# Kernel tuning notes

Measured on AMD Instinct MI355X. Metric: run time of the kernel, lower is better.

The kernel has to match this reference:

```python
import jax, jax.numpy as jnp
import numpy as np

# Geometry constants hardcoded in the torch module
B, H, W = 1, 256, 256
A, DC = 64, 1024            # n_views, det_count
NSAMP = 512                  # samples per ray for the line integral
DSRC, DDET, SPACING = 500.0, 500.0, 2.0
NPAD = 2048                  # fft padding (next pow2 >= 2*DC)
FEAT = 32


def _bilinear_image(img, px, py):
    """Bilinear sample img (B,H,W) at centered coords px,py (any shape). Zero outside."""
    b, hh, ww = img.shape
    cx = px + (ww - 1) / 2.0
    cy = py + (hh - 1) / 2.0
    x0 = jnp.floor(cx); y0 = jnp.floor(cy)
    fx = cx - x0; fy = cy - y0
    x0i = x0.astype(jnp.int32); y0i = y0.astype(jnp.int32)
    flat = img.reshape(b, -1)

    def gather(yi, xi):
        valid = (yi >= 0) & (yi < hh) & (xi >= 0) & (xi < ww)
        yc = jnp.clip(yi, 0, hh - 1); xc = jnp.clip(xi, 0, ww - 1)
        idx = (yc * ww + xc).reshape(-1)
        v = jnp.take(flat, idx, axis=1).reshape((b,) + yi.shape)
        return v * valid.astype(img.dtype)

    return (gather(y0i, x0i) * (1 - fx) * (1 - fy)
            + gather(y0i, x0i + 1) * fx * (1 - fy)
            + gather(y0i + 1, x0i) * (1 - fx) * fy
            + gather(y0i + 1, x0i + 1) * fx * fy)


def fan_forward(img, theta):
    """Ray-driven fan-beam forward projection. img (B,1,H,W) -> sino (B,A,DC)."""
    im = img[:, 0]
    c = jnp.cos(theta); s = jnp.sin(theta)
    src = DSRC * jnp.stack([c, s], -1)                    # (A,2) source positions
    e = jnp.stack([-s, c], -1)                            # detector axis
    u = (jnp.arange(DC) - (DC - 1) / 2.0) * SPACING       # detector offsets
    det = -DDET * jnp.stack([c, s], -1)[:, None, :] + u[None, :, None] * e[:, None, :]  # (A,DC,2)
    d = det - src[:, None, :]
    L = jnp.sqrt(jnp.sum(d * d, axis=-1))                 # (A,DC) ray lengths
    t = (jnp.arange(NSAMP, dtype=jnp.float32) + 0.5) / NSAMP
    pts = src[:, None, None, :] + t[None, None, :, None] * d[:, :, None, :]  # (A,DC,N,2)
    vals = _bilinear_image(im, pts[..., 0], pts[..., 1])  # (B,A,DC,N)
    return jnp.sum(vals, axis=-1) * (L / NSAMP)[None]


def filter_sinogram(sino):
    """Ram-Lak ramp filtering along the detector axis with zero-padding."""
    f = jnp.abs(jnp.fft.rfftfreq(NPAD)).astype(jnp.float32)  # cycles/sample
    sf = jnp.fft.rfft(sino, n=NPAD, axis=-1) * (2.0 * f)
    return jnp.fft.irfft(sf, n=NPAD, axis=-1)[..., :DC].astype(sino.dtype)


def fan_backprojection(sino, theta):
    """Pixel-driven fan-beam backprojection. sino (B,A,DC) -> (B,1,H,W)."""
    xs = jnp.arange(W, dtype=jnp.float32) - (W - 1) / 2.0
    ys = jnp.arange(H, dtype=jnp.float32) - (H - 1) / 2.0
    gx, gy = jnp.meshgrid(xs, ys)                         # (H,W)
    c = jnp.cos(theta)[:, None, None]; s = jnp.sin(theta)[:, None, None]
    xr = gx[None] * c + gy[None] * s                      # (A,H,W) rotated coords
    yr = -gx[None] * s + gy[None] * c
    denom = DSRC - xr
    uu = yr * (DSRC + DDET) / denom                       # detector coordinate
    wgt = (DSRC * DSRC) / (denom * denom)                 # fan-beam distance weight
    iu = uu / SPACING + (DC - 1) / 2.0
    i0 = jnp.floor(iu); fr = iu - i0
    i0i = i0.astype(jnp.int32)
    aidx = jnp.arange(A)[:, None, None]
    b = sino.shape[0]
    flat = sino.reshape(b, -1)

    def g(ii):
        valid = (ii >= 0) & (ii < DC)
        ic = jnp.clip(ii, 0, DC - 1)
        idx = (aidx * DC + ic).reshape(-1)
        v = jnp.take(flat, idx, axis=1).reshape((b, A, H, W))
        return v * valid.astype(sino.dtype)

    vals = g(i0i) * (1 - fr) + g(i0i + 1) * fr            # (B,A,H,W)
    bp = jnp.sum(vals * wgt[None], axis=1) * (jnp.pi / A)
    return bp[:, None]


def conv(x, w):
    return jax.lax.conv_general_dilated(x, w, (1, 1), 'SAME',
                                        dimension_numbers=('NCHW', 'OIHW', 'NCHW'))


def setup_inputs():
    key = jax.random.key(0)
    ks = jax.random.split(key, 8)
    x = jax.random.normal(ks[0], (B, 1, H, W), jnp.float32)
    theta = jnp.arange(A, dtype=jnp.float32) * (2.0 * np.pi / A)
    sinogram = jax.random.normal(ks[1], (B, A, DC), jnp.float32)

    def xav(k, shape):
        fan_in = shape[1] * 9; fan_out = shape[0] * 9
        return jax.random.normal(k, shape, jnp.float32) * np.sqrt(2.0 / (fan_in + fan_out)).astype(np.float32)

    return {
        'x': x, 'theta': theta, 'sinogram': sinogram,
        'lambda_step': jnp.float32(0.5), 'soft_thr': jnp.float32(0.01),
        'conv1_forward': xav(ks[2], (FEAT, 1, 3, 3)),
        'conv2_forward': xav(ks[3], (FEAT, FEAT, 3, 3)),
        'conv1_backward': xav(ks[4], (FEAT, FEAT, 3, 3)),
        'conv2_backward': xav(ks[5], (1, FEAT, 3, 3)),
    }


def reference(x, theta, sinogram, lambda_step, soft_thr,
              conv1_forward, conv2_forward, conv1_backward, conv2_backward):
    sino_pred = fan_forward(x, theta)
    filtered = filter_sinogram(sino_pred)
    X_fbp = fan_backprojection(filtered - sinogram, theta)
    x_input = x - lambda_step * X_fbp
    h = jax.nn.relu(conv(x_input, conv1_forward))
    x_forward = conv(h, conv2_forward)
    hs = jnp.sign(x_forward) * jax.nn.relu(jnp.abs(x_forward) - soft_thr)
    x_pred = conv(jax.nn.relu(conv(hs, conv1_backward)), conv2_backward)
    x_est = conv(jax.nn.relu(conv(x_forward, conv1_backward)), conv2_backward)
    symloss = x_est - x_input
    return (x_pred, symloss)
```

## Files before the change

kernel.cpp:

```cpp
#include <hip/hip_runtime.h>

#define DEV_INLINE __device__ __forceinline__

#define PI_F 3.14159265358979323846f

#define H_OFF     0
#define SINO_OFF  2048
#define DIFF_OFF  67584
#define XIN_OFF   133120
#define WF2F_OFF  198656
#define WF1B_OFF  207872
#define WF2B_OFF  212480
#define BUFA_OFF  217088
#define BUFB_OFF  2314240

typedef short bf16x8 __attribute__((ext_vector_type(8)));
typedef float f32x4 __attribute__((ext_vector_type(4)));

union FragI4 { int4 i4; bf16x8 v; };
union I4U    { int4 i4; int i[4]; };

DEV_INLINE unsigned rne1(float a) {
  unsigned u = __float_as_uint(a);
  return (u + 0x7FFFu + ((u >> 16) & 1u)) >> 16;
}
DEV_INLINE int pack_rne(float a, float b) {
  return (int)(rne1(a) | (rne1(b) << 16));
}

__global__ __launch_bounds__(256) void setup_kernel(
    const float* __restrict__ sino_in, const float* __restrict__ w2f,
    const float* __restrict__ w1b, const float* __restrict__ w2b,
    const float* __restrict__ img,
    float* __restrict__ h, float* __restrict__ diff,
    int* __restrict__ wf2f, int* __restrict__ wf1b, int* __restrict__ wf2b,
    float4* __restrict__ quadP) {
  const int b = blockIdx.x;
  const int tid = threadIdx.x;
  if (b < 64) {
    __shared__ float hp[8][32];
    const int cell = tid & 31;
    const int kq = tid >> 5;
    const int n = b * 32 + cell;
    float ssum = 0.0f;
    const float ang_scale = PI_F / 1024.0f;
    for (int k = kq * 128; k < kq * 128 + 128; ++k) {
      int m = (k * n) & 2047;
      ssum += (float)k * __cosf((float)m * ang_scale);
    }
    hp[kq][cell] = ssum;
    __syncthreads();
    if (tid < 32) {
      float S = 0.0f;
      #pragma unroll
      for (int q = 0; q < 8; ++q) S += hp[q][tid];
      int nn = b * 32 + tid;
      float sgn = (nn & 1) ? -1.0f : 1.0f;
      h[nn] = (S * (1.0f / 512.0f) + sgn) * (1.0f / 2048.0f);
    }
  } else if (b < 320) {
    int idx = (b - 64) * 256 + tid;
    diff[idx] = -sino_in[idx];
  } else if (b < 356) {
    const bool second = (b >= 338);
    int idx = (b - (second ? 338 : 320)) * 256 + tid;
    int d = idx & 3;
    int L = (idx >> 2) & 63;
    int jm = idx >> 8;
    int j = jm >> 1, mt = jm & 1;
    int co = mt * 16 + (L & 15);
    int ci0 = (L >> 4) * 8 + 2 * d;
    const float* w = second ? w1b : w2f;
    int v = pack_rne(w[co * 288 + ci0 * 9 + j], w[co * 288 + (ci0 + 1) * 9 + j]);
    (second ? wf1b : wf2f)[idx] = v;
  } else if (b < 617) {
    int idx = (b - 356) * 256 + tid;
    if (idx < 258 * 258) {
      int y = idx / 258;
      int x = idx - y * 258;
      float4 v;
      int ay = y - 1, bx = x - 1;
      bool y0ok = (ay >= 0 && ay < 256);
      bool y1ok = (ay + 1 >= 0 && ay + 1 < 256);
      bool x0ok = (bx >= 0 && bx < 256);
      bool x1ok = (bx + 1 >= 0 && bx + 1 < 256);
      v.x = (y0ok && x0ok) ? img[(ay << 8) + bx] : 0.0f;
      v.y = (y0ok && x1ok) ? img[(ay << 8) + bx + 1] : 0.0f;
      v.z = (y1ok && x0ok) ? img[((ay + 1) << 8) + bx] : 0.0f;
      v.w = (y1ok && x1ok) ? img[((ay + 1) << 8) + bx + 1] : 0.0f;
      quadP[idx] = v;
    }
  } else {
    int d = tid & 3;
    int L = tid >> 2;
    int n = L & 15;
    int k0 = (L >> 4) * 8 + 2 * d;
    float lo = (n < 9) ? w2b[k0 * 9 + n] : 0.0f;
    float hi = (n < 9) ? w2b[(k0 + 1) * 9 + n] : 0.0f;
    wf2b[tid] = pack_rne(lo, hi);
  }
}

__global__ __launch_bounds__(256) void fwdproj(
    const float4* __restrict__ quadP, const float* __restrict__ theta,
    float* __restrict__ sino) {
  __shared__ float part[8][32];
  __shared__ float cs[2];
  const int tid = threadIdx.x;
  const int a = blockIdx.x >> 5;
  const int cell = tid & 31;
  const int chunk = tid >> 5;
  const int d = ((blockIdx.x & 31) << 5) + cell;
  if (tid == 0) {
    float th = theta[a];
    cs[0] = cosf(th);
    cs[1] = sinf(th);
  }
  __syncthreads();
  const float c = cs[0], s = cs[1];
  const float u = ((float)d - 511.5f) * 2.0f;
  const float dxv = -1000.0f * c - u * s;
  const float dyv = -1000.0f * s + u * c;
  const float L = sqrtf(1.0e6f + u * u);
  const float sx = fmaf(500.0f, c, 127.5f);
  const float sy = fmaf(500.0f, s, 127.5f);

  float tlo = 0.0f, thi = 1.0f;
  if (fabsf(dxv) > 1e-6f) {
    float inv = 1.0f / dxv;
    float a0 = (-1.0f - sx) * inv, a1 = (256.0f - sx) * inv;
    tlo = fmaxf(tlo, fminf(a0, a1));
    thi = fminf(thi, fmaxf(a0, a1));
  } else if (sx <= -1.0f || sx >= 256.0f) {
    thi = -1.0f;
  }
  if (fabsf(dyv) > 1e-6f) {
    float inv = 1.0f / dyv;
    float a0 = (-1.0f - sy) * inv, a1 = (256.0f - sy) * inv;
    tlo = fmaxf(tlo, fminf(a0, a1));
    thi = fminf(thi, fmaxf(a0, a1));
  } else if (sy <= -1.0f || sy >= 256.0f) {
    thi = -1.0f;
  }
  int imin = (int)ceilf(tlo * 512.0f - 0.5f) - 1;
  imin = imin < 0 ? 0 : imin;
  int imax = (int)floorf(thi * 512.0f - 0.5f) + 1;
  imax = imax > 511 ? 511 : imax;

  float acc = 0.0f;
  int i = imin + chunk;
  for (; i + 8 <= imax; i += 16) {
    float t0 = ((float)i + 0.5f) * (1.0f / 512.0f);
    float cx0 = fmaf(t0, dxv, sx);
    float cy0 = fmaf(t0, dyv, sy);
    cx0 = fminf(fmaxf(cx0, -1.0f), 256.0f);
    cy0 = fminf(fmaxf(cy0, -1.0f), 256.0f);
    float xf0 = floorf(cx0), yf0 = floorf(cy0);
    float fx0 = cx0 - xf0, fy0 = cy0 - yf0;
    int idx0 = ((int)yf0 + 1) * 258 + (int)xf0 + 1;
    float t1 = ((float)(i + 8) + 0.5f) * (1.0f / 512.0f);
    float cx1 = fmaf(t1, dxv, sx);
    float cy1 = fmaf(t1, dyv, sy);
    cx1 = fminf(fmaxf(cx1, -1.0f), 256.0f);
    cy1 = fminf(fmaxf(cy1, -1.0f), 256.0f);
    float xf1 = floorf(cx1), yf1 = floorf(cy1);
    float fx1 = cx1 - xf1, fy1 = cy1 - yf1;
    int idx1 = ((int)yf1 + 1) * 258 + (int)xf1 + 1;
    float4 q0 = quadP[idx0];
    float4 q1 = quadP[idx1];
    {
      float gx = 1.0f - fx0, gy = 1.0f - fy0;
      acc += gy * (gx * q0.x + fx0 * q0.y) + fy0 * (gx * q0.z + fx0 * q0.w);
    }
    {
      float gx = 1.0f - fx1, gy = 1.0f - fy1;
      acc += gy * (gx * q1.x + fx1 * q1.y) + fy1 * (gx * q1.z + fx1 * q1.w);
    }
  }
  if (i <= imax) {
    float t = ((float)i + 0.5f) * (1.0f / 512.0f);
    float cx = fmaf(t, dxv, sx);
    float cy = fmaf(t, dyv, sy);
    cx = fminf(fmaxf(cx, -1.0f), 256.0f);
    cy = fminf(fmaxf(cy, -1.0f), 256.0f);
    float xf = floorf(cx), yf = floorf(cy);
    float fx = cx - xf, fy = cy - yf;
    int ix = (int)xf + 1;
    int iy = (int)yf + 1;
    float4 q = quadP[iy * 258 + ix];
    float gx = 1.0f - fx, gy = 1.0f - fy;
    acc += gy * (gx * q.x + fx * q.y) + fy * (gx * q.z + fx * q.w);
  }
  part[chunk][cell] = acc;
  __syncthreads();
  if (tid < 32) {
    float r = 0.0f;
    #pragma unroll
    for (int q = 0; q < 8; ++q) r += part[q][tid];
    sino[a * 1024 + ((blockIdx.x & 31) << 5) + tid] = r * (L * (1.0f / 512.0f));
  }
}

__global__ __launch_bounds__(256) void filt(
    const float* __restrict__ sino_pred, const float* __restrict__ h,
    float* __restrict__ diff) {
  __shared__ __align__(16) float srow[256];
  __shared__ __align__(16) float hextW[1288];
  const int a = blockIdx.x >> 2;
  const int q = blockIdx.x & 3;
  const int tid = threadIdx.x;
  const int k0base = q * 256;
  srow[tid] = sino_pred[a * 1024 + k0base + tid];
  const int shift = 259 + k0base;
  for (int m = tid; m < 1288; m += 256) hextW[m] = h[(m - shift) & 2047];
  __syncthreads();
  const int dd0 = tid * 4;
  float acc0 = 0.f, acc1 = 0.f, acc2 = 0.f, acc3 = 0.f;
  #pragma unroll 4
  for (int kk = 0; kk < 256; kk += 4) {
    float4 sv = *reinterpret_cast<const float4*>(&srow[kk]);
    int mb = dd0 + 256 - kk;
    float4 hA = *reinterpret_cast<const float4*>(&hextW[mb]);
    float4 hB = *reinterpret_cast<const float4*>(&hextW[mb + 4]);
    acc0 = fmaf(sv.x, hA.w, acc0); acc0 = fmaf(sv.y, hA.z, acc0);
    acc0 = fmaf(sv.z, hA.y, acc0); acc0 = fmaf(sv.w, hA.x, acc0);
    acc1 = fmaf(sv.x, hB.x, acc1); acc1 = fmaf(sv.y, hA.w, acc1);
    acc1 = fmaf(sv.z, hA.z, acc1); acc1 = fmaf(sv.w, hA.y, acc1);
    acc2 = fmaf(sv.x, hB.y, acc2); acc2 = fmaf(sv.y, hB.x, acc2);
    acc2 = fmaf(sv.z, hA.w, acc2); acc2 = fmaf(sv.w, hA.z, acc2);
    acc3 = fmaf(sv.x, hB.z, acc3); acc3 = fmaf(sv.y, hB.y, acc3);
    acc3 = fmaf(sv.z, hB.x, acc3); acc3 = fmaf(sv.w, hA.w, acc3);
  }
  float* o = diff + a * 1024 + dd0;
  atomicAdd(o + 0, acc0);
  atomicAdd(o + 1, acc1);
  atomicAdd(o + 2, acc2);
  atomicAdd(o + 3, acc3);
}

__global__ __launch_bounds__(512) void backproj(
    const float* __restrict__ diff, const float* __restrict__ theta,
    const float* __restrict__ lam_p, const float* __restrict__ img,
    float* __restrict__ x_input) {
  __shared__ float cst[64], snt[64];
  __shared__ float part[512];
  const int tid = threadIdx.x;
  if (tid < 64) {
    float th = theta[tid];
    cst[tid] = cosf(th);
    snt[tid] = sinf(th);
  }
  __syncthreads();
  const int tX = (blockIdx.x & 7) << 5;
  const int tY = (blockIdx.x >> 3) << 2;
  const int pl = tid & 127;
  const int ag = tid >> 7;
  const int pxi = tX + (pl & 31);
  const int pyi = tY + (pl >> 5);
  const float gx = (float)pxi - 127.5f;
  const float gy = (float)pyi - 127.5f;
  float acc = 0.0f;
  for (int ai = ag * 16; ai < ag * 16 + 16; ++ai) {
    float c = cst[ai], s = snt[ai];
    float xr = gx * c + gy * s;
    float yr = gy * c - gx * s;
    float denom = 500.0f - xr;
    float inv = 1.0f / denom;
    float uu = yr * 1000.0f * inv;
    float wgt = 250000.0f * inv * inv;
    float iu = uu * 0.5f + 511.5f;
    float i0f = floorf(iu);
    float fr = iu - i0f;
    int i0 = (int)i0f;
    int c0 = min(max(i0, 0), 1023);
    int c1 = min(max(i0 + 1, 0), 1023);
    float m0 = (i0 >= 0 && i0 < 1024) ? 1.0f : 0.0f;
    float m1 = (i0 + 1 >= 0 && i0 + 1 < 1024) ? 1.0f : 0.0f;
    const float* row = diff + ai * 1024;
    float v0 = row[c0] * m0;
    float v1 = row[c1] * m1;
    acc += (v0 * (1.0f - fr) + v1 * fr) * wgt;
  }
  part[tid] = acc;
  __syncthreads();
  if (tid < 128) {
    float sum = part[tid] + part[tid + 128] + part[tid + 256] + part[tid + 384];
    int p = ((tY + (tid >> 5)) << 8) + tX + (tid & 31);
    x_input[p] = img[p] - lam_p[0] * 0.04908738521234052f * sum;
  }
}

__global__ __launch_bounds__(256) void conv12f(
    const float* __restrict__ x_input, const float* __restrict__ w1f,
    const int* __restrict__ wf2f, int* __restrict__ xfp) {
  __shared__ float xin[8][36];
  __shared__ __align__(16) int htile[3264];
  const int tid = threadIdx.x;
  const int lane = tid & 63;
  const int wave = tid >> 6;
  const int tX = (blockIdx.x & 7) << 5;
  const int tY = (blockIdx.x >> 3) << 2;

  FragI4 wf[2][9];
  const int4* wfg = (const int4*)wf2f;
  #pragma unroll
  for (int mt = 0; mt < 2; ++mt)
    #pragma unroll
    for (int j = 0; j < 9; ++j) wf[mt][j].i4 = wfg[(j * 2 + mt) * 64 + lane];

  for (int idx = tid; idx < 288; idx += 256) {
    int sy = idx / 36;
    int sx = idx - sy * 36;
    int gy = tY + sy - 2, gx = tX + sx - 2;
    xin[sy][sx] = (gy >= 0 && gy < 256 && gx >= 0 && gx < 256)
                      ? x_input[(gy << 8) + gx] : 0.0f;
  }
  __syncthreads();

  for (int pos = tid; pos < 204; pos += 256) {
    int yy = pos / 34;
    int xx = pos - yy * 34;
    int hy = tY + yy - 1, hx = tX + xx - 1;
    bool hin = (hy >= 0 && hy < 256 && hx >= 0 && hx < 256);
    float v[9];
    #pragma unroll
    for (int dy = 0; dy < 3; ++dy)
      #pragma unroll
      for (int dx = 0; dx < 3; ++dx) v[dy * 3 + dx] = xin[yy + dy][xx + dx];
    int packs[16];
    #pragma unroll
    for (int c2 = 0; c2 < 16; ++c2) {
      float r0 = 0.0f, r1 = 0.0f;
      #pragma unroll
      for (int j = 0; j < 9; ++j) {
        r0 = fmaf(v[j], w1f[(2 * c2) * 9 + j], r0);
        r1 = fmaf(v[j], w1f[(2 * c2 + 1) * 9 + j], r1);
      }
      r0 = hin ? fmaxf(r0, 0.0f) : 0.0f;
      r1 = hin ? fmaxf(r1, 0.0f) : 0.0f;
      packs[c2] = pack_rne(r0, r1);
    }
    #pragma unroll
    for (int g = 0; g < 4; ++g)
      *reinterpret_cast<int4*>(&htile[g * 816 + pos * 4]) =
          make_int4(packs[4 * g], packs[4 * g + 1],
                    packs[4 * g + 2], packs[4 * g + 3]);
  }
  __syncthreads();

  const int y = wave;
  const int n = lane & 15;
  const int q = lane >> 4;
  const int qb = q * 816;
  for (int xt = 0; xt < 2; ++xt) {
    const int x0 = xt << 4;
    f32x4 acc0 = {0.f, 0.f, 0.f, 0.f};
    f32x4 acc1 = {0.f, 0.f, 0.f, 0.f};
    #pragma unroll
    for (int j = 0; j < 9; ++j) {
      int dy = j / 3, dx = j - dy * 3;
      int pb = (y + dy) * 34 + x0 + dx + n;
      FragI4 bf;
      bf.i4 = *reinterpret_cast<const int4*>(&htile[qb + pb * 4]);
      acc0 = __builtin_amdgcn_mfma_f32_16x16x32_bf16(wf[0][j].v, bf.v, acc0, 0, 0, 0);
      acc1 = __builtin_amdgcn_mfma_f32_16x16x32_bf16(wf[1][j].v, bf.v, acc1, 0, 0, 0);
    }
    const int gpos = ((tY + y) << 8) + tX + x0 + n;
    int2* xp = (int2*)(xfp + (gpos << 4));
    xp[q]     = make_int2(pack_rne(acc0[0], acc0[1]), pack_rne(acc0[2], acc0[3]));
    xp[4 + q] = make_int2(pack_rne(acc1[0], acc1[1]), pack_rne(acc1[2], acc1[3]));
  }
}

__global__ __launch_bounds__(256) void branch_tail(
    const int* __restrict__ xfp, const int* __restrict__ wf1b,
    const int* __restrict__ wf2b, const float* __restrict__ thr_p,
    const float* __restrict__ x_input, float* __restrict__ out) {
  __shared__ __align__(16) int ldsX[8704];
  __shared__ __align__(16) int ldsD[6400];
  float* ldsP = (float*)ldsX;
  const int tid = threadIdx.x;
  const int lane = tid & 63;
  const int wave = tid >> 6;
  const int branch = blockIdx.x >> 8;
  const int tileb = blockIdx.x & 255;
  const int tX = (tileb & 3) << 6;
  const int tY = (tileb >> 2) << 2;
  const float thr = thr_p[0];
  const bool soft = (branch == 0);

  FragI4 wf[2][9];
  const int4* wfg = (const int4*)wf1b;
  #pragma unroll
  for (int mt = 0; mt < 2; ++mt)
    #pragma unroll
    for (int j = 0; j < 9; ++j) wf[mt][j].i4 = wfg[(j * 2 + mt) * 64 + lane];
  FragI4 wb;
  wb.i4 = ((const int4*)wf2b)[lane];

  if (tid < 16) {
    int g = tid >> 2, px = 396 + (tid & 3);
    *reinterpret_cast<int4*>(&ldsD[g * 1600 + px * 4]) = make_int4(0, 0, 0, 0);
  }

  #pragma unroll
  for (int t = 0; t < 3; ++t) {
    int p = tid + t * 256;
    if (p < 544) {
      int sy = p / 68;
      int sx = p - sy * 68;
      int gy = tY + sy - 2, gx = tX + sx - 2;
      bool ok = ((unsigned)gy < 256u) && ((unsigned)gx < 256u);
      I4U w[4];
      if (ok) {
        const int4* src = (const int4*)(xfp + (((gy << 8) + gx) << 4));
        w[0].i4 = src[0]; w[1].i4 = src[1]; w[2].i4 = src[2]; w[3].i4 = src[3];
      } else {
        w[0].i4 = w[1].i4 = w[2].i4 = w[3].i4 = make_int4(0, 0, 0, 0);
      }
      #pragma unroll
      for (int g = 0; g < 4; ++g) {
        if (soft) {
          #pragma unroll
          for (int k = 0; k < 4; ++k) {
            int v = w[g].i[k];
            float lo = __uint_as_float(((unsigned)v) << 16);
            float hi = __uint_as_float(((unsigned)v) & 0xFFFF0000u);
            lo = fmaxf(lo - thr, 0.0f) + fminf(lo + thr, 0.0f);
            hi = fmaxf(hi - thr, 0.0f) + fminf(hi + thr, 0.0f);
            w[g].i[k] = pack_rne(lo, hi);
          }
        }
        *reinterpret_cast<int4*>(&ldsX[g * 2176 + p * 4]) = w[g].i4;
      }
    }
  }
  __syncthreads();

  const int n = lane & 15;
  const int q = lane >> 4;
  const int rxtab[5] = {-1, 15, 31, 47, 49};
  for (int t = wave; t < 30; t += 4) {
    int trow = t / 5;
    int ry = trow - 1;
    int rx0 = rxtab[t - trow * 5];
    int rxn = rx0 + n;
    bool inimg = ((unsigned)(tX + rxn) < 256u) && ((unsigned)(tY + ry) < 256u);
    int pxD = (ry + 1) * 66 + rxn + 1;
    f32x4 acc0 = {0.f, 0.f, 0.f, 0.f};
    f32x4 acc1 = {0.f, 0.f, 0.f, 0.f};
    #pragma unroll
    for (int j = 0; j < 9; ++j) {
      int dy = j / 3, dx = j - dy * 3;
      int pb = (ry + 1 + dy) * 68 + rx0 + 1 + dx + n;
      FragI4 bf;
      bf.i4 = *reinterpret_cast<const int4*>(&ldsX[q * 2176 + pb * 4]);
      acc0 = __builtin_amdgcn_mfma_f32_16x16x32_bf16(wf[0][j].v, bf.v, acc0, 0, 0, 0);
      acc1 = __builtin_amdgcn_mfma_f32_16x16x32_bf16(wf[1][j].v, bf.v, acc1, 0, 0, 0);
    }
    float a00 = inimg ? fmaxf(acc0[0], 0.0f) : 0.0f;
    float a01 = inimg ? fmaxf(acc0[1], 0.0f) : 0.0f;
    float a02 = inimg ? fmaxf(acc0[2], 0.0f) : 0.0f;
    float a03 = inimg ? fmaxf(acc0[3], 0.0f) : 0.0f;
    float a10 = inimg ? fmaxf(acc1[0], 0.0f) : 0.0f;
    float a11 = inimg ? fmaxf(acc1[1], 0.0f) : 0.0f;
    float a12 = inimg ? fmaxf(acc1[2], 0.0f) : 0.0f;
    float a13 = inimg ? fmaxf(acc1[3], 0.0f) : 0.0f;
    *reinterpret_cast<int2*>(
        &ldsD[(q >> 1) * 1600 + pxD * 4 + (q & 1) * 2]) =
        make_int2(pack_rne(a00, a01), pack_rne(a02, a03));
    *reinterpret_cast<int2*>(
        &ldsD[(2 + (q >> 1)) * 1600 + pxD * 4 + (q & 1) * 2]) =
        make_int2(pack_rne(a10, a11), pack_rne(a12, a13));
  }
  __syncthreads();

  for (int t = wave; t < 25; t += 4) {
    int pbase = t << 4;
    FragI4 af;
    af.i4 = *reinterpret_cast<const int4*>(&ldsD[q * 1600 + (pbase + n) * 4]);
    f32x4 acc = {0.f, 0.f, 0.f, 0.f};
    acc = __builtin_amdgcn_mfma_f32_16x16x32_bf16(af.v, wb.v, acc, 0, 0, 0);
    #pragma unroll
    for (int r = 0; r < 4; ++r)
      ldsP[(pbase + q * 4 + r) * 17 + n] = acc[r];
  }
  __syncthreads();

  const int px = tid & 63, py = tid >> 6;
  float acc = 0.0f;
  #pragma unroll
  for (int j = 0; j < 9; ++j) {
    int dy = j / 3, dx = j - dy * 3;
    int rp = (py + dy) * 66 + px + dx;
    acc += ldsP[rp * 17 + j];
  }
  const int p = ((tY + py) << 8) + tX + px;
  if (branch == 0) out[p] = acc;
  else out[65536 + p] = acc - x_input[p];
}

extern "C" void kernel_launch(void* const* d_in, const int* in_sizes, int n_in,
                              void* d_out, int out_size, void* d_ws, size_t ws_size,
                              hipStream_t stream) {
  const float* x       = (const float*)d_in[0];
  const float* theta   = (const float*)d_in[1];
  const float* sino_in = (const float*)d_in[2];
  const float* lam     = (const float*)d_in[3];
  const float* thr     = (const float*)d_in[4];
  const float* w_c1f   = (const float*)d_in[5];
  const float* w_c2f   = (const float*)d_in[6];
  const float* w_c1b   = (const float*)d_in[7];
  const float* w_c2b   = (const float*)d_in[8];
  float* out = (float*)d_out;
  float* ws  = (float*)d_ws;

  float* h         = ws + H_OFF;
  float* sino_pred = ws + SINO_OFF;
  float* diff      = ws + DIFF_OFF;
  float* x_input   = ws + XIN_OFF;
  int*   wf2f      = (int*)(ws + WF2F_OFF);
  int*   wf1b      = (int*)(ws + WF1B_OFF);
  int*   wf2b      = (int*)(ws + WF2B_OFF);
  float4* quadP    = (float4*)(ws + BUFA_OFF);
  int*   xfp       = (int*)(ws + BUFB_OFF);

  setup_kernel<<<618, 256, 0, stream>>>(sino_in, w_c2f, w_c1b, w_c2b, x, h,
                                        diff, wf2f, wf1b, wf2b, quadP);
  fwdproj<<<2048, 256, 0, stream>>>(quadP, theta, sino_pred);
  filt<<<256, 256, 0, stream>>>(sino_pred, h, diff);
  backproj<<<512, 512, 0, stream>>>(diff, theta, lam, x, x_input);
  conv12f<<<512, 256, 0, stream>>>(x_input, w_c1f, wf2f, xfp);
  branch_tail<<<512, 256, 0, stream>>>(xfp, wf1b, wf2b, thr, x_input, out);
}
```

Before: 127.4 us.

## Fuse filter, backprojection and conv stages into one cooperative kernel with grid syncs

Replaces the four tail kernels (ramp filter, backprojection, first conv pair, branch tail) with a single cooperative kernel of 256 blocks of 512 threads that separates stages with grid.sync(). Each block now handles two tiles per stage, and both branches are processed sequentially within a block. The goal is to remove kernel launch gaps and per-kernel ramp overhead. In exchange it drops to 256 blocks, leaves half the threads idle in some phases, and carries grid-barrier cost plus a large shared-memory footprint that limits occupancy.

Result: slower. 226.3 us (+77.7%).

```diff
diff --git a/kernel.cpp b/kernel.cpp
--- a/kernel.cpp
+++ b/kernel.cpp
@@ -1,7 +1,9 @@
 #include <hip/hip_runtime.h>
+#include <hip/hip_cooperative_groups.h>
+
+namespace cg = cooperative_groups;
 
 #define DEV_INLINE __device__ __forceinline__
-
 #define PI_F 3.14159265358979323846f
 
 #define H_OFF     0
@@ -201,303 +203,326 @@
   }
 }
 
-__global__ __launch_bounds__(256) void filt(
-    const float* __restrict__ sino_pred, const float* __restrict__ h,
-    float* __restrict__ diff) {
-  __shared__ __align__(16) float srow[256];
-  __shared__ __align__(16) float hextW[1288];
-  const int a = blockIdx.x >> 2;
-  const int q = blockIdx.x & 3;
+__global__ __launch_bounds__(512) void fused_tail(
+    const float* __restrict__ img, const float* __restrict__ theta,
+    const float* __restrict__ lam_p, const float* __restrict__ thr_p,
+    const float* __restrict__ w1f, const int* __restrict__ wf2f,
+    const int* __restrict__ wf1b, const int* __restrict__ wf2b,
+    const float* __restrict__ hbuf, const float* __restrict__ sino,
+    float* __restrict__ diff, float* __restrict__ x_input,
+    int* __restrict__ xfp, float* __restrict__ out) {
+  __shared__ __align__(16) int U[15104];
+  cg::grid_group grid = cg::this_grid();
+  const int b = blockIdx.x;
   const int tid = threadIdx.x;
-  const int k0base = q * 256;
-  srow[tid] = sino_pred[a * 1024 + k0base + tid];
-  const int shift = 259 + k0base;
-  for (int m = tid; m < 1288; m += 256) hextW[m] = h[(m - shift) & 2047];
-  __syncthreads();
-  const int dd0 = tid * 4;
-  float acc0 = 0.f, acc1 = 0.f, acc2 = 0.f, acc3 = 0.f;
-  #pragma unroll 4
-  for (int kk = 0; kk < 256; kk += 4) {
-    float4 sv = *reinterpret_cast<const float4*>(&srow[kk]);
-    int mb = dd0 + 256 - kk;
-    float4 hA = *reinterpret_cast<const float4*>(&hextW[mb]);
-    float4 hB = *reinterpret_cast<const float4*>(&hextW[mb + 4]);
-    acc0 = fmaf(sv.x, hA.w, acc0); acc0 = fmaf(sv.y, hA.z, acc0);
-    acc0 = fmaf(sv.z, hA.y, acc0); acc0 = fmaf(sv.w, hA.x, acc0);
-    acc1 = fmaf(sv.x, hB.x, acc1); acc1 = fmaf(sv.y, hA.w, acc1);
-    acc1 = fmaf(sv.z, hA.z, acc1); acc1 = fmaf(sv.w, hA.y, acc1);
-    acc2 = fmaf(sv.x, hB.y, acc2); acc2 = fmaf(sv.y, hB.x, acc2);
-    acc2 = fmaf(sv.z, hA.w, acc2); acc2 = fmaf(sv.w, hA.z, acc2);
-    acc3 = fmaf(sv.x, hB.z, acc3); acc3 = fmaf(sv.y, hB.y, acc3);
-    acc3 = fmaf(sv.z, hB.x, acc3); acc3 = fmaf(sv.w, hA.w, acc3);
-  }
-  float* o = diff + a * 1024 + dd0;
-  atomicAdd(o + 0, acc0);
-  atomicAdd(o + 1, acc1);
-  atomicAdd(o + 2, acc2);
-  atomicAdd(o + 3, acc3);
-}
-
-__global__ __launch_bounds__(512) void backproj(
-    const float* __restrict__ diff, const float* __restrict__ theta,
-    const float* __restrict__ lam_p, const float* __restrict__ img,
-    float* __restrict__ x_input) {
-  __shared__ float cst[64], snt[64];
-  __shared__ float part[512];
-  const int tid = threadIdx.x;
-  if (tid < 64) {
-    float th = theta[tid];
-    cst[tid] = cosf(th);
-    snt[tid] = sinf(th);
-  }
-  __syncthreads();
-  const int tX = (blockIdx.x & 7) << 5;
-  const int tY = (blockIdx.x >> 3) << 2;
-  const int pl = tid & 127;
-  const int ag = tid >> 7;
-  const int pxi = tX + (pl & 31);
-  const int pyi = tY + (pl >> 5);
-  const float gx = (float)pxi - 127.5f;
-  const float gy = (float)pyi - 127.5f;
-  float acc = 0.0f;
-  for (int ai = ag * 16; ai < ag * 16 + 16; ++ai) {
-    float c = cst[ai], s = snt[ai];
-    float xr = gx * c + gy * s;
-    float yr = gy * c - gx * s;
-    float denom = 500.0f - xr;
-    float inv = 1.0f / denom;
-    float uu = yr * 1000.0f * inv;
-    float wgt = 250000.0f * inv * inv;
-    float iu = uu * 0.5f + 511.5f;
-    float i0f = floorf(iu);
-    float fr = iu - i0f;
-    int i0 = (int)i0f;
-    int c0 = min(max(i0, 0), 1023);
-    int c1 = min(max(i0 + 1, 0), 1023);
-    float m0 = (i0 >= 0 && i0 < 1024) ? 1.0f : 0.0f;
-    float m1 = (i0 + 1 >= 0 && i0 + 1 < 1024) ? 1.0f : 0.0f;
-    const float* row = diff + ai * 1024;
-    float v0 = row[c0] * m0;
-    float v1 = row[c1] * m1;
-    acc += (v0 * (1.0f - fr) + v1 * fr) * wgt;
-  }
-  part[tid] = acc;
-  __syncthreads();
-  if (tid < 128) {
-    float sum = part[tid] + part[tid + 128] + part[tid + 256] + part[tid + 384];
-    int p = ((tY + (tid >> 5)) << 8) + tX + (tid & 31);
-    x_input[p] = img[p] - lam_p[0] * 0.04908738521234052f * sum;
-  }
-}
-
-__global__ __launch_bounds__(256) void conv12f(
-    const float* __restrict__ x_input, const float* __restrict__ w1f,
-    const int* __restrict__ wf2f, int* __restrict__ xfp) {
-  __shared__ float xin[8][36];
-  __shared__ __align__(16) int htile[3264];
-  const int tid = threadIdx.x;
-  const int lane = tid & 63;
-  const int wave = tid >> 6;
-  const int tX = (blockIdx.x & 7) << 5;
-  const int tY = (blockIdx.x >> 3) << 2;
-
-  FragI4 wf[2][9];
-  const int4* wfg = (const int4*)wf2f;
-  #pragma unroll
-  for (int mt = 0; mt < 2; ++mt)
+
+  {
+    float* srow  = (float*)U;
+    float* hextW = (float*)U + 256;
+    const int a = b >> 2;
+    const int q = b & 3;
+    const int k0base = q * 256;
+    if (tid < 256) srow[tid] = sino[a * 1024 + k0base + tid];
+    const int shift = 259 + k0base;
+    for (int m = tid; m < 1288; m += 512) hextW[m] = hbuf[(m - shift) & 2047];
+    __syncthreads();
+    if (tid < 256) {
+      const int dd0 = tid * 4;
+      float acc0 = 0.f, acc1 = 0.f, acc2 = 0.f, acc3 = 0.f;
+      #pragma unroll 4
+      for (int kk = 0; kk < 256; kk += 4) {
+        float4 sv = *reinterpret_cast<const float4*>(&srow[kk]);
+        int mb = dd0 + 256 - kk;
+        float4 hA = *reinterpret_cast<const float4*>(&hextW[mb]);
+        float4 hB = *reinterpret_cast<const float4*>(&hextW[mb + 4]);
+        acc0 = fmaf(sv.x, hA.w, acc0); acc0 = fmaf(sv.y, hA.z, acc0);
+        acc0 = fmaf(sv.z, hA.y, acc0); acc0 = fmaf(sv.w, hA.x, acc0);
+        acc1 = fmaf(sv.x, hB.x, acc1); acc1 = fmaf(sv.y, hA.w, acc1);
+        acc1 = fmaf(sv.z, hA.z, acc1); acc1 = fmaf(sv.w, hA.y, acc1);
+        acc2 = fmaf(sv.x, hB.y, acc2); acc2 = fmaf(sv.y, hB.x, acc2);
+        acc2 = fmaf(sv.z, hA.w, acc2); acc2 = fmaf(sv.w, hA.z, acc2);
+        acc3 = fmaf(sv.x, hB.z, acc3); acc3 = fmaf(sv.y, hB.y, acc3);
+        acc3 = fmaf(sv.z, hB.x, acc3); acc3 = fmaf(sv.w, hA.w, acc3);
+      }
+      float* o = diff + a * 1024 + dd0;
+      atomicAdd(o + 0, acc0);
+      atomicAdd(o + 1, acc1);
+      atomicAdd(o + 2, acc2);
+      atomicAdd(o + 3, acc3);
+    }
+  }
+  grid.sync();
+
+  {
+    float* cst  = (float*)U;
+    float* snt  = (float*)U + 64;
+    float* part = (float*)U + 128;
+    if (tid < 64) {
+      float th = theta[tid];
+      cst[tid] = cosf(th);
+      snt[tid] = sinf(th);
+    }
+    __syncthreads();
+    const int tX = (b & 7) << 5;
+    const int tYb = (b >> 3) << 3;
+    const int pl = tid & 127;
+    const int ag = tid >> 7;
+    const float lamc = lam_p[0] * 0.04908738521234052f;
     #pragma unroll
-    for (int j = 0; j < 9; ++j) wf[mt][j].i4 = wfg[(j * 2 + mt) * 64 + lane];
-
-  for (int idx = tid; idx < 288; idx += 256) {
-    int sy = idx / 36;
-    int sx = idx - sy * 36;
-    int gy = tY + sy - 2, gx = tX + sx - 2;
-    xin[sy][sx] = (gy >= 0 && gy < 256 && gx >= 0 && gx < 256)
-                      ? x_input[(gy << 8) + gx] : 0.0f;
-  }
-  __syncthreads();
-
-  for (int pos = tid; pos < 204; pos += 256) {
-    int yy = pos / 34;
-    int xx = pos - yy * 34;
-    int hy = tY + yy - 1, hx = tX + xx - 1;
-    bool hin = (hy >= 0 && hy < 256 && hx >= 0 && hx < 256);
-    float v[9];
+    for (int tt = 0; tt < 2; ++tt) {
+      const int tY = tYb + (tt << 2);
+      const int pxi = tX + (pl & 31);
+      const int pyi = tY + (pl >> 5);
+      const float gx = (float)pxi - 127.5f;
+      const float gy = (float)pyi - 127.5f;
+      float acc = 0.0f;
+      for (int ai = ag * 16; ai < ag * 16 + 16; ++ai) {
+        float c = cst[ai], s = snt[ai];
+        float xr = gx * c + gy * s;
+        float yr = gy * c - gx * s;
+        float denom = 500.0f - xr;
+        float inv = 1.0f / denom;
+        float uu = yr * 1000.0f * inv;
+        float wgt = 250000.0f * inv * inv;
+        float iu = uu * 0.5f + 511.5f;
+        float i0f = floorf(iu);
+        float fr = iu - i0f;
+        int i0 = (int)i0f;
+        int c0 = min(max(i0, 0), 1023);
+        int c1 = min(max(i0 + 1, 0), 1023);
+        float m0 = (i0 >= 0 && i0 < 1024) ? 1.0f : 0.0f;
+        float m1 = (i0 + 1 >= 0 && i0 + 1 < 1024) ? 1.0f : 0.0f;
+        const float* row = diff + ai * 1024;
+        float v0 = row[c0] * m0;
+        float v1 = row[c1] * m1;
+        acc += (v0 * (1.0f - fr) + v1 * fr) * wgt;
+      }
+      part[tid] = acc;
+      __syncthreads();
+      if (tid < 128) {
+        float sum = part[tid] + part[tid + 128] + part[tid + 256] + part[tid + 384];
+        int p = ((tY + (tid >> 5)) << 8) + tX + (tid & 31);
+        x_input[p] = img[p] - lamc * sum;
+      }
+      __syncthreads();
+    }
+  }
+  grid.sync();
+
+  {
+    float (*xin)[36] = (float(*)[36])U;
+    int* htile = U + 288;
+    const int lane = tid & 63;
+    const int wave = tid >> 6;
+    const int tX = (b & 7) << 5;
+    const int tYb = (b >> 3) << 3;
+
+    FragI4 wfr[2][9];
+    const int4* wfg = (const int4*)wf2f;
     #pragma unroll
-    for (int dy = 0; dy < 3; ++dy)
+    for (int mt = 0; mt < 2; ++mt)
       #pragma unroll
-      for (int dx = 0; dx < 3; ++dx) v[dy * 3 + dx] = xin[yy + dy][xx + dx];
-    int packs[16];
+      for (int j = 0; j < 9; ++j) wfr[mt][j].i4 = wfg[(j * 2 + mt) * 64 + lane];
+
     #pragma unroll
-    for (int c2 = 0; c2 < 16; ++c2) {
-      float r0 = 0.0f, r1 = 0.0f;
+    for (int tt = 0; tt < 2; ++tt) {
+      const int tY = tYb + (tt << 2);
+      if (tid < 288) {
+        int sy = tid / 36;
+        int sx = tid - sy * 36;
+        int gy = tY + sy - 2, gx = tX + sx - 2;
+        xin[sy][sx] = (gy >= 0 && gy < 256 && gx >= 0 && gx < 256)
+                          ? x_input[(gy << 8) + gx] : 0.0f;
+      }
+      __syncthreads();
+
+      if (tid < 204) {
+        int pos = tid;
+        int yy = pos / 34;
+        int xx = pos - yy * 34;
+        int hy = tY + yy - 1, hx = tX + xx - 1;
+        bool hin = (hy >= 0 && hy < 256 && hx >= 0 && hx < 256);
+        float v[9];
+        #pragma unroll
+        for (int dy = 0; dy < 3; ++dy)
+          #pragma unroll
+          for (int dx = 0; dx < 3; ++dx) v[dy * 3 + dx] = xin[yy + dy][xx + dx];
+        int packs[16];
+        #pragma unroll
+        for (int c2 = 0; c2 < 16; ++c2) {
+          float r0 = 0.0f, r1 = 0.0f;
+          #pragma unroll
+          for (int j = 0; j < 9; ++j) {
+            r0 = fmaf(v[j], w1f[(2 * c2) * 9 + j], r0);
+            r1 = fmaf(v[j], w1f[(2 * c2 + 1) * 9 + j], r1);
+          }
+          r0 = hin ? fmaxf(r0, 0.0f) : 0.0f;
+          r1 = hin ? fmaxf(r1, 0.0f) : 0.0f;
+          packs[c2] = pack_rne(r0, r1);
+        }
+        #pragma unroll
+        for (int g = 0; g < 4; ++g)
+          *reinterpret_cast<int4*>(&htile[g * 816 + pos * 4]) =
+              make_int4(packs[4 * g], packs[4 * g + 1],
+                        packs[4 * g + 2], packs[4 * g + 3]);
+      }
+      __syncthreads();
+
+      {
+        const int y = wave & 3;
+        const int xt = wave >> 2;
+        const int n = lane & 15;
+        const int q = lane >> 4;
+        const int qb = q * 816;
+        const int x0 = xt << 4;
+        f32x4 acc0 = {0.f, 0.f, 0.f, 0.f};
+        f32x4 acc1 = {0.f, 0.f, 0.f, 0.f};
+        #pragma unroll
+        for (int j = 0; j < 9; ++j) {
+          int dy = j / 3, dx = j - dy * 3;
+          int pb = (y + dy) * 34 + x0 + dx + n;
+          FragI4 bf;
+          bf.i4 = *reinterpret_cast<const int4*>(&htile[qb + pb * 4]);
+          acc0 = __builtin_amdgcn_mfma_f32_16x16x32_bf16(wfr[0][j].v, bf.v, acc0, 0, 0, 0);
+          acc1 = __builtin_amdgcn_mfma_f32_16x16x32_bf16(wfr[1][j].v, bf.v, acc1, 0, 0, 0);
+        }
+        const int gpos = ((tY + y) << 8) + tX + x0 + n;
+        int2* xp = (int2*)(xfp + (gpos << 4));
+        xp[q]     = make_int2(pack_rne(acc0[0], acc0[1]), pack_rne(acc0[2], acc0[3]));
+        xp[4 + q] = make_int2(pack_rne(acc1[0], acc1[1]), pack_rne(acc1[2], acc1[3]));
+      }
+      __syncthreads();
+    }
+  }
+  grid.sync();
+
+  {
+    int* ldsX = U;
+    int* ldsD = U + 8704;
+    float* ldsP = (float*)U;
+    const int lane = tid & 63;
+    const int wave = tid >> 6;
+    const int tX = (b & 3) << 6;
+    const int tY = (b >> 2) << 2;
+    const float thr = thr_p[0];
+
+    FragI4 wfr[2][9];
+    const int4* wfg = (const int4*)wf1b;
+    #pragma unroll
+    for (int mt = 0; mt < 2; ++mt)
       #pragma unroll
-      for (int j = 0; j < 9; ++j) {
-        r0 = fmaf(v[j], w1f[(2 * c2) * 9 + j], r0);
-        r1 = fmaf(v[j], w1f[(2 * c2 + 1) * 9 + j], r1);
-      }
-      r0 = hin ? fmaxf(r0, 0.0f) : 0.0f;
-      r1 = hin ? fmaxf(r1, 0.0f) : 0.0f;
-      packs[c2] = pack_rne(r0, r1);
-    }
-    #pragma unroll
-    for (int g = 0; g < 4; ++g)
-      *reinterpret_cast<int4*>(&htile[g * 816 + pos * 4]) =
-          make_int4(packs[4 * g], packs[4 * g + 1],
-                    packs[4 * g + 2], packs[4 * g + 3]);
-  }
-  __syncthreads();
-
-  const int y = wave;
-  const int n = lane & 15;
-  const int q = lane >> 4;
-  const int qb = q * 816;
-  for (int xt = 0; xt < 2; ++xt) {
-    const int x0 = xt << 4;
-    f32x4 acc0 = {0.f, 0.f, 0.f, 0.f};
-    f32x4 acc1 = {0.f, 0.f, 0.f, 0.f};
-    #pragma unroll
-    for (int j = 0; j < 9; ++j) {
-      int dy = j / 3, dx = j - dy * 3;
-      int pb = (y + dy) * 34 + x0 + dx + n;
-      FragI4 bf;
-      bf.i4 = *reinterpret_cast<const int4*>(&htile[qb + pb * 4]);
-      acc0 = __builtin_amdgcn_mfma_f32_16x16x32_bf16(wf[0][j].v, bf.v, acc0, 0, 0, 0);
-      acc1 = __builtin_amdgcn_mfma_f32_16x16x32_bf16(wf[1][j].v, bf.v, acc1, 0, 0, 0);
-    }
-    const int gpos = ((tY + y) << 8) + tX + x0 + n;
-    int2* xp = (int2*)(xfp + (gpos << 4));
-    xp[q]     = make_int2(pack_rne(acc0[0], acc0[1]), pack_rne(acc0[2], acc0[3]));
-    xp[4 + q] = make_int2(pack_rne(acc1[0], acc1[1]), pack_rne(acc1[2], acc1[3]));
-  }
-}
-
-__global__ __launch_bounds__(256) void branch_tail(
-    const int* __restrict__ xfp, const int* __restrict__ wf1b,
-    const int* __restrict__ wf2b, const float* __restrict__ thr_p,
-    const float* __restrict__ x_input, float* __restrict__ out) {
-  __shared__ __align__(16) int ldsX[8704];
-  __shared__ __align__(16) int ldsD[6400];
-  float* ldsP = (float*)ldsX;
-  const int tid = threadIdx.x;
-  const int lane = tid & 63;
-  const int wave = tid >> 6;
-  const int branch = blockIdx.x >> 8;
-  const int tileb = blockIdx.x & 255;
-  const int tX = (tileb & 3) << 6;
-  const int tY = (tileb >> 2) << 2;
-  const float thr = thr_p[0];
-  const bool soft = (branch == 0);
-
-  FragI4 wf[2][9];
-  const int4* wfg = (const int4*)wf1b;
-  #pragma unroll
-  for (int mt = 0; mt < 2; ++mt)
-    #pragma unroll
-    for (int j = 0; j < 9; ++j) wf[mt][j].i4 = wfg[(j * 2 + mt) * 64 + lane];
-  FragI4 wb;
-  wb.i4 = ((const int4*)wf2b)[lane];
-
-  if (tid < 16) {
-    int g = tid >> 2, px = 396 + (tid & 3);
-    *reinterpret_cast<int4*>(&ldsD[g * 1600 + px * 4]) = make_int4(0, 0, 0, 0);
-  }
-
-  #pragma unroll
-  for (int t = 0; t < 3; ++t) {
-    int p = tid + t * 256;
-    if (p < 544) {
-      int sy = p / 68;
-      int sx = p - sy * 68;
-      int gy = tY + sy - 2, gx = tX + sx - 2;
-      bool ok = ((unsigned)gy < 256u) && ((unsigned)gx < 256u);
-      I4U w[4];
-      if (ok) {
-        const int4* src = (const int4*)(xfp + (((gy << 8) + gx) << 4));
-        w[0].i4 = src[0]; w[1].i4 = src[1]; w[2].i4 = src[2]; w[3].i4 = src[3];
-      } else {
-        w[0].i4 = w[1].i4 = w[2].i4 = w[3].i4 = make_int4(0, 0, 0, 0);
-      }
+      for (int j = 0; j < 9; ++j) wfr[mt][j].i4 = wfg[(j * 2 + mt) * 64 + lane];
+    FragI4 wb;
+    wb.i4 = ((const int4*)wf2b)[lane];
+
+    if (tid < 16) {
+      int g = tid >> 2, px = 396 + (tid & 3);
+      *reinterpret_cast<int4*>(&ldsD[g * 1600 + px * 4]) = make_int4(0, 0, 0, 0);
+    }
+
+    const int n = lane & 15;
+    const int q = lane >> 4;
+    const int rxtab[5] = {-1, 15, 31, 47, 49};
+
+    for (int bb = 0; bb < 2; ++bb) {
+      const bool soft = (bb == 0);
       #pragma unroll
-      for (int g = 0; g < 4; ++g) {
-        if (soft) {
+      for (int t = 0; t < 2; ++t) {
+        int p = tid + t * 512;
+        if (p < 544) {
+          int sy = p / 68;
+          int sx = p - sy * 68;
+          int gy = tY + sy - 2, gx = tX + sx - 2;
+          bool ok = ((unsigned)gy < 256u) && ((unsigned)gx < 256u);
+          I4U w[4];
+          if (ok) {
+            const int4* src = (const int4*)(xfp + (((gy << 8) + gx) << 4));
+            w[0].i4 = src[0]; w[1].i4 = src[1]; w[2].i4 = src[2]; w[3].i4 = src[3];
+          } else {
+            w[0].i4 = w[1].i4 = w[2].i4 = w[3].i4 = make_int4(0, 0, 0, 0);
+          }
           #pragma unroll
-          for (int k = 0; k < 4; ++k) {
-            int v = w[g].i[k];
-            float lo = __uint_as_float(((unsigned)v) << 16);
-            float hi = __uint_as_float(((unsigned)v) & 0xFFFF0000u);
-            lo = fmaxf(lo - thr, 0.0f) + fminf(lo + thr, 0.0f);
-            hi = fmaxf(hi - thr, 0.0f) + fminf(hi + thr, 0.0f);
-            w[g].i[k] = pack_rne(lo, hi);
+          for (int g = 0; g < 4; ++g) {
+            if (soft) {
+              #pragma unroll
+              for (int k = 0; k < 4; ++k) {
+                int v = w[g].i[k];
+                float lo = __uint_as_float(((unsigned)v) << 16);
+                float hi = __uint_as_float(((unsigned)v) & 0xFFFF0000u);
+                lo = fmaxf(lo - thr, 0.0f) + fminf(lo + thr, 0.0f);
+                hi = fmaxf(hi - thr, 0.0f) + fminf(hi + thr, 0.0f);
+                w[g].i[k] = pack_rne(lo, hi);
+              }
+            }
+            *reinterpret_cast<int4*>(&ldsX[g * 2176 + p * 4]) = w[g].i4;
           }
         }
-        *reinterpret_cast<int4*>(&ldsX[g * 2176 + p * 4]) = w[g].i4;
-      }
-    }
-  }
-  __syncthreads();
-
-  const int n = lane & 15;
-  const int q = lane >> 4;
-  const int rxtab[5] = {-1, 15, 31, 47, 49};
-  for (int t = wave; t < 30; t += 4) {
-    int trow = t / 5;
-    int ry = trow - 1;
-    int rx0 = rxtab[t - trow * 5];
-    int rxn = rx0 + n;
-    bool inimg = ((unsigned)(tX + rxn) < 256u) && ((unsigned)(tY + ry) < 256u);
-    int pxD = (ry + 1) * 66 + rxn + 1;
-    f32x4 acc0 = {0.f, 0.f, 0.f, 0.f};
-    f32x4 acc1 = {0.f, 0.f, 0.f, 0.f};
-    #pragma unroll
-    for (int j = 0; j < 9; ++j) {
-      int dy = j / 3, dx = j - dy * 3;
-      int pb = (ry + 1 + dy) * 68 + rx0 + 1 + dx + n;
-      FragI4 bf;
-      bf.i4 = *reinterpret_cast<const int4*>(&ldsX[q * 2176 + pb * 4]);
-      acc0 = __builtin_amdgcn_mfma_f32_16x16x32_bf16(wf[0][j].v, bf.v, acc0, 0, 0, 0);
-      acc1 = __builtin_amdgcn_mfma_f32_16x16x32_bf16(wf[1][j].v, bf.v, acc1, 0, 0, 0);
-    }
-    float a00 = inimg ? fmaxf(acc0[0], 0.0f) : 0.0f;
-    float a01 = inimg ? fmaxf(acc0[1], 0.0f) : 0.0f;
-    float a02 = inimg ? fmaxf(acc0[2], 0.0f) : 0.0f;
-    float a03 = inimg ? fmaxf(acc0[3], 0.0f) : 0.0f;
-    float a10 = inimg ? fmaxf(acc1[0], 0.0f) : 0.0f;
-    float a11 = inimg ? fmaxf(acc1[1], 0.0f) : 0.0f;
-    float a12 = inimg ? fmaxf(acc1[2], 0.0f) : 0.0f;
-    float a13 = inimg ? fmaxf(acc1[3], 0.0f) : 0.0f;
-    *reinterpret_cast<int2*>(
-        &ldsD[(q >> 1) * 1600 + pxD * 4 + (q & 1) * 2]) =
-        make_int2(pack_rne(a00, a01), pack_rne(a02, a03));
-    *reinterpret_cast<int2*>(
-        &ldsD[(2 + (q >> 1)) * 1600 + pxD * 4 + (q & 1) * 2]) =
-        make_int2(pack_rne(a10, a11), pack_rne(a12, a13));
-  }
-  __syncthreads();
-
-  for (int t = wave; t < 25; t += 4) {
-    int pbase = t << 4;
-    FragI4 af;
-    af.i4 = *reinterpret_cast<const int4*>(&ldsD[q * 1600 + (pbase + n) * 4]);
-    f32x4 acc = {0.f, 0.f, 0.f, 0.f};
-    acc = __builtin_amdgcn_mfma_f32_16x16x32_bf16(af.v, wb.v, acc, 0, 0, 0);
-    #pragma unroll
-    for (int r = 0; r < 4; ++r)
-      ldsP[(pbase + q * 4 + r) * 17 + n] = acc[r];
-  }
-  __syncthreads();
-
-  const int px = tid & 63, py = tid >> 6;
-  float acc = 0.0f;
-  #pragma unroll
-  for (int j = 0; j < 9; ++j) {
-    int dy = j / 3, dx = j - dy * 3;
-    int rp = (py + dy) * 66 + px + dx;
-    acc += ldsP[rp * 17 + j];
-  }
-  const int p = ((tY + py) << 8) + tX + px;
-  if (branch == 0) out[p] = acc;
-  else out[65536 + p] = acc - x_input[p];
+      }
+      __syncthreads();
+
+      for (int t = wave; t < 30; t += 8) {
+        int trow = t / 5;
+        int ry = trow - 1;
+        int rx0 = rxtab[t - trow * 5];
+        int rxn = rx0 + n;
+        bool inimg = ((unsigned)(tX + rxn) < 256u) && ((unsigned)(tY + ry) < 256u);
+        int pxD = (ry + 1) * 66 + rxn + 1;
+        f32x4 acc0 = {0.f, 0.f, 0.f, 0.f};
+        f32x4 acc1 = {0.f, 0.f, 0.f, 0.f};
+        #pragma unroll
+        for (int j = 0; j < 9; ++j) {
+          int dy = j / 3, dx = j - dy * 3;
+          int pb = (ry + 1 + dy) * 68 + rx0 + 1 + dx + n;
+          FragI4 bf;
+          bf.i4 = *reinterpret_cast<const int4*>(&ldsX[q * 2176 + pb * 4]);
+          acc0 = __builtin_amdgcn_mfma_f32_16x16x32_bf16(wfr[0][j].v, bf.v, acc0, 0, 0, 0);
+          acc1 = __builtin_amdgcn_mfma_f32_16x16x32_bf16(wfr[1][j].v, bf.v, acc1, 0, 0, 0);
+        }
+        float a00 = inimg ? fmaxf(acc0[0], 0.0f) : 0.0f;
+        float a01 = inimg ? fmaxf(acc0[1], 0.0f) : 0.0f;
+        float a02 = inimg ? fmaxf(acc0[2], 0.0f) : 0.0f;
+        float a03 = inimg ? fmaxf(acc0[3], 0.0f) : 0.0f;
+        float a10 = inimg ? fmaxf(acc1[0], 0.0f) : 0.0f;
+        float a11 = inimg ? fmaxf(acc1[1], 0.0f) : 0.0f;
+        float a12 = inimg ? fmaxf(acc1[2], 0.0f) : 0.0f;
+        float a13 = inimg ? fmaxf(acc1[3], 0.0f) : 0.0f;
+        *reinterpret_cast<int2*>(
+            &ldsD[(q >> 1) * 1600 + pxD * 4 + (q & 1) * 2]) =
+            make_int2(pack_rne(a00, a01), pack_rne(a02, a03));
+        *reinterpret_cast<int2*>(
+            &ldsD[(2 + (q >> 1)) * 1600 + pxD * 4 + (q & 1) * 2]) =
+            make_int2(pack_rne(a10, a11), pack_rne(a12, a13));
+      }
+      __syncthreads();
+
+      for (int t = wave; t < 25; t += 8) {
+        int pbase = t << 4;
+        FragI4 af;
+        af.i4 = *reinterpret_cast<const int4*>(&ldsD[q * 1600 + (pbase + n) * 4]);
+        f32x4 acc = {0.f, 0.f, 0.f, 0.f};
+        acc = __builtin_amdgcn_mfma_f32_16x16x32_bf16(af.v, wb.v, acc, 0, 0, 0);
+        #pragma unroll
+        for (int r = 0; r < 4; ++r)
+          ldsP[(pbase + q * 4 + r) * 17 + n] = acc[r];
+      }
+      __syncthreads();
+
+      if (tid < 256) {
+        const int px = tid & 63, py = tid >> 6;
+        float acc = 0.0f;
+        #pragma unroll
+        for (int j = 0; j < 9; ++j) {
+          int dy = j / 3, dx = j - dy * 3;
+          int rp = (py + dy) * 66 + px + dx;
+          acc += ldsP[rp * 17 + j];
+        }
+        const int p = ((tY + py) << 8) + tX + px;
+        if (bb == 0) out[p] = acc;
+        else out[65536 + p] = acc - x_input[p];
+      }
+      __syncthreads();
+    }
+  }
 }
 
 extern "C" void kernel_launch(void* const* d_in, const int* in_sizes, int n_in,
@@ -528,8 +553,11 @@
   setup_kernel<<<618, 256, 0, stream>>>(sino_in, w_c2f, w_c1b, w_c2b, x, h,
                                         diff, wf2f, wf1b, wf2b, quadP);
   fwdproj<<<2048, 256, 0, stream>>>(quadP, theta, sino_pred);
-  filt<<<256, 256, 0, stream>>>(sino_pred, h, diff);
-  backproj<<<512, 512, 0, stream>>>(diff, theta, lam, x, x_input);
-  conv12f<<<512, 256, 0, stream>>>(x_input, w_c1f, wf2f, xfp);
-  branch_tail<<<512, 256, 0, stream>>>(xfp, wf1b, wf2b, thr, x_input, out);
+
+  void* args[] = {(void*)&x, (void*)&theta, (void*)&lam, (void*)&thr,
+                  (void*)&w_c1f, (void*)&wf2f, (void*)&wf1b, (void*)&wf2b,
+                  (void*)&h, (void*)&sino_pred, (void*)&diff, (void*)&x_input,
+                  (void*)&xfp, (void*)&out};
+  hipLaunchCooperativeKernel((const void*)fused_tail, dim3(256), dim3(512),
+                             args, 0, stream);
 }
```
